# Kernel optimization log

Hardware: AMD Instinct MI355X
Metric: run time of the kernel (lower is better)

Reference implementation:

```python
import jax, jax.numpy as jnp
import numpy as np

N_NODES = 100000
N_EDGES = 1200000
N_GRAPHS = 1024
IN_DIM, HIDDEN, OUT_DIM = 4, 64, 2
BN_EPS = 1e-5


def setup_inputs() -> dict:
    key = jax.random.key(0)
    ks = jax.random.split(key, 12)
    x = jax.random.normal(ks[0], (N_NODES, IN_DIM), dtype=jnp.float32)
    edge_index = jax.random.randint(ks[1], (2, N_EDGES), 0, N_NODES, dtype=jnp.int64)
    batch = jnp.sort(jax.random.randint(ks[2], (N_NODES,), 0, N_GRAPHS, dtype=jnp.int64))
    s = 1.0 / np.sqrt(HIDDEN)
    return {
        "x": x,
        "edge_index": edge_index,
        "batch": batch,
        "W_enc": jax.random.normal(ks[3], (IN_DIM, HIDDEN), dtype=jnp.float32) * 0.5,
        "b_enc": jnp.zeros((HIDDEN,), dtype=jnp.float32),
        "bn_gamma": jnp.ones((HIDDEN,), dtype=jnp.float32),
        "bn_beta": jnp.zeros((HIDDEN,), dtype=jnp.float32),
        "bn_mean": jax.random.normal(ks[4], (HIDDEN,), dtype=jnp.float32) * 0.1,
        "bn_var": jax.random.uniform(ks[5], (HIDDEN,), dtype=jnp.float32, minval=0.5, maxval=1.5),
        "W_gcn": jax.random.normal(ks[6], (HIDDEN, HIDDEN), dtype=jnp.float32) * s,
        "b_gcn": jnp.zeros((HIDDEN,), dtype=jnp.float32),
        "W_cls1": jax.random.normal(ks[7], (HIDDEN, HIDDEN), dtype=jnp.float32) * s,
        "b_cls1": jnp.zeros((HIDDEN,), dtype=jnp.float32),
        "W_cls2": jax.random.normal(ks[8], (HIDDEN, OUT_DIM), dtype=jnp.float32) * s,
        "b_cls2": jnp.zeros((OUT_DIM,), dtype=jnp.float32),
    }


def reference(x, edge_index, batch, W_enc, b_enc, bn_gamma, bn_beta, bn_mean, bn_var,
              W_gcn, b_gcn, W_cls1, b_cls1, W_cls2, b_cls2):
    n = x.shape[0]
    # Encoder: Linear -> ReLU -> Dropout(eval=identity) -> BatchNorm1d (running stats)
    h = jnp.maximum(x @ W_enc + b_enc, 0.0)
    h = (h - bn_mean) * jax.lax.rsqrt(bn_var + BN_EPS) * bn_gamma + bn_beta
    # GCNConv (PyG): add self-loops, symmetric deg^{-1/2} normalization
    loop = jnp.arange(n, dtype=edge_index.dtype)
    src = jnp.concatenate([edge_index[0], loop])  # [E+N]
    dst = jnp.concatenate([edge_index[1], loop])
    deg = jnp.zeros((n,), dtype=h.dtype).at[dst].add(1.0)
    dis = jnp.where(deg > 0, jax.lax.rsqrt(jnp.maximum(deg, 1.0)), 0.0)
    norm = dis[src] * dis[dst]  # [E+N]
    hw = h @ W_gcn  # [N, H]
    msg = hw[src] * norm[:, None]  # gather + scale, [E+N, H]
    agg = jax.ops.segment_sum(msg, dst, num_segments=n) + b_gcn
    agg = jnp.maximum(agg, 0.0)  # .relu()
    # global_mean_pool over graphs
    sums = jax.ops.segment_sum(agg, batch, num_segments=N_GRAPHS)  # [G, H]
    cnts = jax.ops.segment_sum(jnp.ones((n,), dtype=agg.dtype), batch, num_segments=N_GRAPHS)
    gm = sums / jnp.maximum(cnts, 1.0)[:, None]
    # Classifier: Linear -> ReLU -> Dropout(eval) -> Linear
    out = jnp.maximum(gm @ W_cls1 + b_cls1, 0.0) @ W_cls2 + b_cls2
    return out
```

## Files before the change

### kernel.cpp

```cpp
#include <hip/hip_runtime.h>

#define N_NODES  100000
#define N_EDGES  1200000
#define N_GRAPHS 1024

#define BSH    8
#define BNODES 256
#define NBUCK  391
#define BCAP   4096
#define BINB   512
#define CHUNK  ((N_EDGES + BINB - 1) / BINB)
#define ENCB   1563

__device__ __forceinline__ unsigned short f2bf(float f) {
  unsigned u = __float_as_uint(f);
  return (unsigned short)((u + 0x7fffu + ((u >> 16) & 1u)) >> 16);
}
__device__ __forceinline__ float bf2f(unsigned short b) {
  return __uint_as_float(((unsigned)b) << 16);
}

__global__ __launch_bounds__(256) void k_zero(float* __restrict__ gsum,
                                              int* __restrict__ cur,
                                              const int* __restrict__ batch,
                                              float* __restrict__ cnts) {
  int i = blockIdx.x * 256 + threadIdx.x;
  gsum[i] = 0.f;
  if (i < NBUCK) cur[i] = 0;
  if (i < N_GRAPHS) {
    int lo = 0, hi = N_NODES;
    while (lo < hi) { int mid = (lo + hi) >> 1; if (batch[mid] < i) lo = mid + 1; else hi = mid; }
    int lo2 = lo, hi2 = N_NODES;
    while (lo2 < hi2) { int mid = (lo2 + hi2) >> 1; if (batch[mid] < i + 1) lo2 = mid + 1; else hi2 = mid; }
    cnts[i] = fmaxf((float)(lo2 - lo), 1.0f);
  }
}

__global__ __launch_bounds__(256, 2) void k_binenc(
    const int* __restrict__ ei, int* __restrict__ cur, int* __restrict__ binned,
    const float* __restrict__ x,
    const float* __restrict__ Wenc, const float* __restrict__ benc,
    const float* __restrict__ gamma, const float* __restrict__ beta,
    const float* __restrict__ mean,  const float* __restrict__ var,
    const float* __restrict__ Wgcn,
    unsigned short* __restrict__ hw) {
  int t = threadIdx.x;
  int lane = t & 63, w = t >> 6;
  if (blockIdx.x < BINB) {
    __shared__ int h[NBUCK];
    int blk = blockIdx.x;
    for (int i = t; i < NBUCK; i += 256) h[i] = 0;
    __syncthreads();
    int start = blk * CHUNK, end = min(start + CHUNK, N_EDGES);
    for (int e = start + 4 * t; e < end; e += 4 * 256) {
      int4 d4 = *(const int4*)&ei[N_EDGES + e];
      atomicAdd(&h[d4.x >> BSH], 1);
      atomicAdd(&h[d4.y >> BSH], 1);
      atomicAdd(&h[d4.z >> BSH], 1);
      atomicAdd(&h[d4.w >> BSH], 1);
    }
    __syncthreads();
    for (int b = t; b < NBUCK; b += 256) {
      int v = h[b];
      if (v) h[b] = atomicAdd(&cur[b], v);
    }
    __syncthreads();
    for (int e = start + 4 * t; e < end; e += 4 * 256) {
      int4 s4 = *(const int4*)&ei[e];
      int4 d4 = *(const int4*)&ei[N_EDGES + e];
      int b, p;
      b = d4.x >> BSH; p = atomicAdd(&h[b], 1);
      if (p < BCAP) binned[b * BCAP + p] = s4.x | ((d4.x & (BNODES - 1)) << 17);
      b = d4.y >> BSH; p = atomicAdd(&h[b], 1);
      if (p < BCAP) binned[b * BCAP + p] = s4.y | ((d4.y & (BNODES - 1)) << 17);
      b = d4.z >> BSH; p = atomicAdd(&h[b], 1);
      if (p < BCAP) binned[b * BCAP + p] = s4.z | ((d4.z & (BNODES - 1)) << 17);
      b = d4.w >> BSH; p = atomicAdd(&h[b], 1);
      if (p < BCAP) binned[b * BCAP + p] = s4.w | ((d4.w & (BNODES - 1)) << 17);
    }
    return;
  }
  int wv = (blockIdx.x - BINB) * 4 + w;
  if (wv >= 6250) return;
  float be = benc[lane];
  float sc = gamma[lane] * rsqrtf(var[lane] + 1e-5f);
  float mu = mean[lane], bt = beta[lane];
  float w0 = Wenc[lane], w1 = Wenc[64 + lane], w2 = Wenc[128 + lane], w3 = Wenc[192 + lane];
  float wreg[64];
  #pragma unroll
  for (int k = 0; k < 64; ++k) wreg[k] = Wgcn[k * 64 + lane];
  int n0 = wv * 16;
  for (int i = 0; i < 16; ++i) {
    int n = n0 + i;
    float4 xv = ((const float4*)x)[n];
    float h = fmaf(xv.w, w3, fmaf(xv.z, w2, fmaf(xv.y, w1, fmaf(xv.x, w0, be))));
    h = fmaxf(h, 0.f);
    float hbn = (h - mu) * sc + bt;
    int hb = __float_as_int(hbn);
    float a0 = 0.f, a1 = 0.f, a2 = 0.f, a3 = 0.f;
    #pragma unroll
    for (int k = 0; k < 64; k += 4) {
      a0 = fmaf(__int_as_float(__builtin_amdgcn_readlane(hb, k)),     wreg[k],     a0);
      a1 = fmaf(__int_as_float(__builtin_amdgcn_readlane(hb, k + 1)), wreg[k + 1], a1);
      a2 = fmaf(__int_as_float(__builtin_amdgcn_readlane(hb, k + 2)), wreg[k + 2], a2);
      a3 = fmaf(__int_as_float(__builtin_amdgcn_readlane(hb, k + 3)), wreg[k + 3], a3);
    }
    hw[(size_t)n * 64 + lane] = f2bf((a0 + a1) + (a2 + a3));
  }
}

__global__ __launch_bounds__(256) void k_csr(const int* __restrict__ cur,
                                             const int* __restrict__ binned,
                                             int* __restrict__ csr,
                                             unsigned* __restrict__ rowinfo,
                                             float* __restrict__ dis) {
  __shared__ int hist[BNODES];
  __shared__ int wsum[4];
  int t = threadIdx.x, blk = blockIdx.x;
  int lane = t & 63, w = t >> 6;
  int nE = min(cur[blk], BCAP);
  int b0 = blk * BCAP;
  hist[t] = 0;
  __syncthreads();
  for (int i = t; i < nE; i += 256)
    atomicAdd(&hist[(unsigned)binned[b0 + i] >> 17], 1);
  __syncthreads();
  int v = hist[t];
  int incl = v;
  #pragma unroll
  for (int off = 1; off < 64; off <<= 1) {
    int y = __shfl_up(incl, off);
    if (lane >= off) incl += y;
  }
  if (lane == 63) wsum[w] = incl;
  __syncthreads();
  if (t == 0) {
    int s = 0;
    #pragma unroll
    for (int i = 0; i < 4; ++i) { int x2 = wsum[i]; wsum[i] = s; s += x2; }
  }
  __syncthreads();
  int excl = wsum[w] + incl - v;
  hist[t] = excl;
  int node = (blk << BSH) + t;
  if (node < N_NODES) {
    rowinfo[node] = (unsigned)(b0 + excl) | ((unsigned)v << 21);
    dis[node] = rsqrtf((float)(v + 1));
  }
  __syncthreads();
  for (int i = t; i < nE; i += 256) {
    int vv = binned[b0 + i];
    int p = atomicAdd(&hist[(unsigned)vv >> 17], 1);
    csr[b0 + p] = vv & 0x1FFFF;
  }
}

__global__ __launch_bounds__(256) void k_gather(
    const unsigned* __restrict__ rowinfo, const int* __restrict__ csr,
    const float* __restrict__ dis, const unsigned short* __restrict__ hw,
    const int* __restrict__ batch, const float* __restrict__ bgcn,
    float* __restrict__ gsum) {
  int t = threadIdx.x;
  int lane = t & 63, w = t >> 6;
  int nb = blockIdx.x * 16 + w * 4;
  float bias = bgcn[lane];
  float vout[4];
  int gid[4];
  #pragma unroll
  for (int k = 0; k < 4; ++k) {
    int n = nb + k;
    unsigned u = rowinfo[n];
    int st = (int)(u & 0x1FFFFF);
    int v  = (int)(u >> 21);
    int en = st + v;
    float dn = rsqrtf((float)(v + 1));
    float a0 = 0.f, a1 = 0.f, a2 = 0.f, a3 = 0.f;
    float a4 = 0.f, a5 = 0.f, a6 = 0.f, a7 = 0.f;
    for (int c = st; c < en; c += 64) {
      int m = min(64, en - c);
      int idx = c + lane;
      int chunk = 0; float dv = 0.f;
      if (idx < en) { chunk = csr[idx]; dv = dis[chunk]; }
      int dvb = __float_as_int(dv);
      int j = 0;
      for (; j + 8 <= m; j += 8) {
        int s0 = __builtin_amdgcn_readlane(chunk, j);
        int s1 = __builtin_amdgcn_readlane(chunk, j + 1);
        int s2 = __builtin_amdgcn_readlane(chunk, j + 2);
        int s3 = __builtin_amdgcn_readlane(chunk, j + 3);
        int s4 = __builtin_amdgcn_readlane(chunk, j + 4);
        int s5 = __builtin_amdgcn_readlane(chunk, j + 5);
        int s6 = __builtin_amdgcn_readlane(chunk, j + 6);
        int s7 = __builtin_amdgcn_readlane(chunk, j + 7);
        float d0 = __int_as_float(__builtin_amdgcn_readlane(dvb, j));
        float d1 = __int_as_float(__builtin_amdgcn_readlane(dvb, j + 1));
        float d2 = __int_as_float(__builtin_amdgcn_readlane(dvb, j + 2));
        float d3 = __int_as_float(__builtin_amdgcn_readlane(dvb, j + 3));
        float d4 = __int_as_float(__builtin_amdgcn_readlane(dvb, j + 4));
        float d5 = __int_as_float(__builtin_amdgcn_readlane(dvb, j + 5));
        float d6 = __int_as_float(__builtin_amdgcn_readlane(dvb, j + 6));
        float d7 = __int_as_float(__builtin_amdgcn_readlane(dvb, j + 7));
        a0 = fmaf(d0, bf2f(hw[(size_t)s0 * 64 + lane]), a0);
        a1 = fmaf(d1, bf2f(hw[(size_t)s1 * 64 + lane]), a1);
        a2 = fmaf(d2, bf2f(hw[(size_t)s2 * 64 + lane]), a2);
        a3 = fmaf(d3, bf2f(hw[(size_t)s3 * 64 + lane]), a3);
        a4 = fmaf(d4, bf2f(hw[(size_t)s4 * 64 + lane]), a4);
        a5 = fmaf(d5, bf2f(hw[(size_t)s5 * 64 + lane]), a5);
        a6 = fmaf(d6, bf2f(hw[(size_t)s6 * 64 + lane]), a6);
        a7 = fmaf(d7, bf2f(hw[(size_t)s7 * 64 + lane]), a7);
      }
      for (; j + 4 <= m; j += 4) {
        int s0 = __builtin_amdgcn_readlane(chunk, j);
        int s1 = __builtin_amdgcn_readlane(chunk, j + 1);
        int s2 = __builtin_amdgcn_readlane(chunk, j + 2);
        int s3 = __builtin_amdgcn_readlane(chunk, j + 3);
        float d0 = __int_as_float(__builtin_amdgcn_readlane(dvb, j));
        float d1 = __int_as_float(__builtin_amdgcn_readlane(dvb, j + 1));
        float d2 = __int_as_float(__builtin_amdgcn_readlane(dvb, j + 2));
        float d3 = __int_as_float(__builtin_amdgcn_readlane(dvb, j + 3));
        a0 = fmaf(d0, bf2f(hw[(size_t)s0 * 64 + lane]), a0);
        a1 = fmaf(d1, bf2f(hw[(size_t)s1 * 64 + lane]), a1);
        a2 = fmaf(d2, bf2f(hw[(size_t)s2 * 64 + lane]), a2);
        a3 = fmaf(d3, bf2f(hw[(size_t)s3 * 64 + lane]), a3);
      }
      for (; j < m; ++j) {
        int s = __builtin_amdgcn_readlane(chunk, j);
        float d = __int_as_float(__builtin_amdgcn_readlane(dvb, j));
        a0 = fmaf(d, bf2f(hw[(size_t)s * 64 + lane]), a0);
      }
    }
    float self = bf2f(hw[(size_t)n * 64 + lane]);
    float sum = ((a0 + a1) + (a2 + a3)) + ((a4 + a5) + (a6 + a7));
    vout[k] = fmaxf(dn * fmaf(dn, self, sum) + bias, 0.f);
    gid[k] = batch[n];
  }
  float vs = vout[0];
  int cg = gid[0];
  #pragma unroll
  for (int k = 1; k < 4; ++k) {
    if (gid[k] == cg) vs += vout[k];
    else {
      atomicAdd(&gsum[cg * 64 + lane], vs);
      vs = vout[k]; cg = gid[k];
    }
  }
  atomicAdd(&gsum[cg * 64 + lane], vs);
}

__global__ void k_cls(const float* __restrict__ gsum, const float* __restrict__ cnts,
                      const float* __restrict__ W1, const float* __restrict__ b1,
                      const float* __restrict__ W2, const float* __restrict__ b2,
                      float* __restrict__ out) {
  __shared__ float gm[64];
  int j = threadIdx.x;
  int g = blockIdx.x;
  gm[j] = gsum[g * 64 + j] / cnts[g];
  __syncthreads();
  float hid = b1[j];
  #pragma unroll
  for (int k = 0; k < 64; ++k) hid += gm[k] * W1[k * 64 + j];
  hid = fmaxf(hid, 0.f);
  float o0 = hid * W2[j * 2 + 0];
  float o1 = hid * W2[j * 2 + 1];
  #pragma unroll
  for (int off = 32; off > 0; off >>= 1) {
    o0 += __shfl_down(o0, off);
    o1 += __shfl_down(o1, off);
  }
  if (j == 0) {
    out[g * 2 + 0] = o0 + b2[0];
    out[g * 2 + 1] = o1 + b2[1];
  }
}

extern "C" void kernel_launch(void* const* d_in, const int* in_sizes, int n_in,
                              void* d_out, int out_size, void* d_ws, size_t ws_size,
                              hipStream_t stream) {
  const float* x     = (const float*)d_in[0];
  const int*   ei    = (const int*)d_in[1];
  const int*   batch = (const int*)d_in[2];
  const float* Wenc  = (const float*)d_in[3];
  const float* benc  = (const float*)d_in[4];
  const float* gamma = (const float*)d_in[5];
  const float* beta  = (const float*)d_in[6];
  const float* mean  = (const float*)d_in[7];
  const float* var   = (const float*)d_in[8];
  const float* Wgcn  = (const float*)d_in[9];
  const float* bgcn  = (const float*)d_in[10];
  const float* W1    = (const float*)d_in[11];
  const float* b1    = (const float*)d_in[12];
  const float* W2    = (const float*)d_in[13];
  const float* b2    = (const float*)d_in[14];
  float* out = (float*)d_out;

  char* ws = (char*)d_ws;
  float*          gsum    = (float*)ws;          ws += (size_t)N_GRAPHS * 64 * 4;
  int*            cur     = (int*)ws;            ws += (size_t)1024 * 4;
  float*          cnts    = (float*)ws;          ws += (size_t)N_GRAPHS * 4;
  int*            binned  = (int*)ws;            ws += (size_t)NBUCK * BCAP * 4;
  int*            csr     = (int*)ws;            ws += (size_t)NBUCK * BCAP * 4;
  unsigned*       rowinfo = (unsigned*)ws;       ws += (size_t)(N_NODES + 32) * 4;
  float*          dis     = (float*)ws;          ws += (size_t)N_NODES * 4;
  unsigned short* hw      = (unsigned short*)ws; ws += (size_t)N_NODES * 64 * 2;

  k_zero<<<256, 256, 0, stream>>>(gsum, cur, batch, cnts);
  k_binenc<<<BINB + ENCB, 256, 0, stream>>>(ei, cur, binned, x, Wenc, benc,
                                            gamma, beta, mean, var, Wgcn, hw);
  k_csr<<<NBUCK, 256, 0, stream>>>(cur, binned, csr, rowinfo, dis);
  k_gather<<<(N_NODES / 16), 256, 0, stream>>>(rowinfo, csr, dis, hw, batch, bgcn, gsum);
  k_cls<<<N_GRAPHS, 64, 0, stream>>>(gsum, cnts, W1, b1, W2, b2, out);
}
```

Measured before the change: 193.8 us.

## Prescale hw rows by source deg^-1/2 in CSR build, drop dis gather

The source-side normalization factor is folded into hw inside k_csr: each block rescales its 256 nodes' bf16 rows by rsqrt(deg+1) once. The gather kernel then only sums the prescaled rows, which removes the dependent dis[chunk] load and the per-edge readlane/fma of the scale. The gather unroll also drops from 8 to 4 accumulators. In exchange, k_csr does an extra read-modify-write of the whole hw array, and each row is rounded to bf16 a second time, which adds precision error.

After: 208.5 us. 7.6% more time.

```diff
diff --git a/kernel.cpp b/kernel.cpp
--- a/kernel.cpp
+++ b/kernel.cpp
@@ -113,8 +113,9 @@
                                              const int* __restrict__ binned,
                                              int* __restrict__ csr,
                                              unsigned* __restrict__ rowinfo,
-                                             float* __restrict__ dis) {
+                                             unsigned short* __restrict__ hw) {
   __shared__ int hist[BNODES];
+  __shared__ float disS[BNODES];
   __shared__ int wsum[4];
   int t = threadIdx.x, blk = blockIdx.x;
   int lane = t & 63, w = t >> 6;
@@ -142,12 +143,19 @@
   __syncthreads();
   int excl = wsum[w] + incl - v;
   hist[t] = excl;
+  disS[t] = rsqrtf((float)(v + 1));
   int node = (blk << BSH) + t;
-  if (node < N_NODES) {
+  if (node < N_NODES)
     rowinfo[node] = (unsigned)(b0 + excl) | ((unsigned)v << 21);
-    dis[node] = rsqrtf((float)(v + 1));
-  }
-  __syncthreads();
+  __syncthreads();
+  int base = blk << BSH;
+  for (int r = w * 64; r < w * 64 + 64; ++r) {
+    int n = base + r;
+    if (n >= N_NODES) break;
+    float d = disS[r];
+    size_t off = (size_t)n * 64 + lane;
+    hw[off] = f2bf(bf2f(hw[off]) * d);
+  }
   for (int i = t; i < nE; i += 256) {
     int vv = binned[b0 + i];
     int p = atomicAdd(&hist[(unsigned)vv >> 17], 1);
@@ -157,7 +165,7 @@
 
 __global__ __launch_bounds__(256) void k_gather(
     const unsigned* __restrict__ rowinfo, const int* __restrict__ csr,
-    const float* __restrict__ dis, const unsigned short* __restrict__ hw,
+    const unsigned short* __restrict__ hw,
     const int* __restrict__ batch, const float* __restrict__ bgcn,
     float* __restrict__ gsum) {
   int t = threadIdx.x;
@@ -175,63 +183,29 @@
     int en = st + v;
     float dn = rsqrtf((float)(v + 1));
     float a0 = 0.f, a1 = 0.f, a2 = 0.f, a3 = 0.f;
-    float a4 = 0.f, a5 = 0.f, a6 = 0.f, a7 = 0.f;
     for (int c = st; c < en; c += 64) {
       int m = min(64, en - c);
       int idx = c + lane;
-      int chunk = 0; float dv = 0.f;
-      if (idx < en) { chunk = csr[idx]; dv = dis[chunk]; }
-      int dvb = __float_as_int(dv);
+      int chunk = (idx < en) ? csr[idx] : 0;
       int j = 0;
-      for (; j + 8 <= m; j += 8) {
-        int s0 = __builtin_amdgcn_readlane(chunk, j);
-        int s1 = __builtin_amdgcn_readlane(chunk, j + 1);
-        int s2 = __builtin_amdgcn_readlane(chunk, j + 2);
-        int s3 = __builtin_amdgcn_readlane(chunk, j + 3);
-        int s4 = __builtin_amdgcn_readlane(chunk, j + 4);
-        int s5 = __builtin_amdgcn_readlane(chunk, j + 5);
-        int s6 = __builtin_amdgcn_readlane(chunk, j + 6);
-        int s7 = __builtin_amdgcn_readlane(chunk, j + 7);
-        float d0 = __int_as_float(__builtin_amdgcn_readlane(dvb, j));
-        float d1 = __int_as_float(__builtin_amdgcn_readlane(dvb, j + 1));
-        float d2 = __int_as_float(__builtin_amdgcn_readlane(dvb, j + 2));
-        float d3 = __int_as_float(__builtin_amdgcn_readlane(dvb, j + 3));
-        float d4 = __int_as_float(__builtin_amdgcn_readlane(dvb, j + 4));
-        float d5 = __int_as_float(__builtin_amdgcn_readlane(dvb, j + 5));
-        float d6 = __int_as_float(__builtin_amdgcn_readlane(dvb, j + 6));
-        float d7 = __int_as_float(__builtin_amdgcn_readlane(dvb, j + 7));
-        a0 = fmaf(d0, bf2f(hw[(size_t)s0 * 64 + lane]), a0);
-        a1 = fmaf(d1, bf2f(hw[(size_t)s1 * 64 + lane]), a1);
-        a2 = fmaf(d2, bf2f(hw[(size_t)s2 * 64 + lane]), a2);
-        a3 = fmaf(d3, bf2f(hw[(size_t)s3 * 64 + lane]), a3);
-        a4 = fmaf(d4, bf2f(hw[(size_t)s4 * 64 + lane]), a4);
-        a5 = fmaf(d5, bf2f(hw[(size_t)s5 * 64 + lane]), a5);
-        a6 = fmaf(d6, bf2f(hw[(size_t)s6 * 64 + lane]), a6);
-        a7 = fmaf(d7, bf2f(hw[(size_t)s7 * 64 + lane]), a7);
-      }
       for (; j + 4 <= m; j += 4) {
         int s0 = __builtin_amdgcn_readlane(chunk, j);
         int s1 = __builtin_amdgcn_readlane(chunk, j + 1);
         int s2 = __builtin_amdgcn_readlane(chunk, j + 2);
         int s3 = __builtin_amdgcn_readlane(chunk, j + 3);
-        float d0 = __int_as_float(__builtin_amdgcn_readlane(dvb, j));
-        float d1 = __int_as_float(__builtin_amdgcn_readlane(dvb, j + 1));
-        float d2 = __int_as_float(__builtin_amdgcn_readlane(dvb, j + 2));
-        float d3 = __int_as_float(__builtin_amdgcn_readlane(dvb, j + 3));
-        a0 = fmaf(d0, bf2f(hw[(size_t)s0 * 64 + lane]), a0);
-        a1 = fmaf(d1, bf2f(hw[(size_t)s1 * 64 + lane]), a1);
-        a2 = fmaf(d2, bf2f(hw[(size_t)s2 * 64 + lane]), a2);
-        a3 = fmaf(d3, bf2f(hw[(size_t)s3 * 64 + lane]), a3);
+        a0 += bf2f(hw[(size_t)s0 * 64 + lane]);
+        a1 += bf2f(hw[(size_t)s1 * 64 + lane]);
+        a2 += bf2f(hw[(size_t)s2 * 64 + lane]);
+        a3 += bf2f(hw[(size_t)s3 * 64 + lane]);
       }
       for (; j < m; ++j) {
         int s = __builtin_amdgcn_readlane(chunk, j);
-        float d = __int_as_float(__builtin_amdgcn_readlane(dvb, j));
-        a0 = fmaf(d, bf2f(hw[(size_t)s * 64 + lane]), a0);
+        a0 += bf2f(hw[(size_t)s * 64 + lane]);
       }
     }
     float self = bf2f(hw[(size_t)n * 64 + lane]);
-    float sum = ((a0 + a1) + (a2 + a3)) + ((a4 + a5) + (a6 + a7));
-    vout[k] = fmaxf(dn * fmaf(dn, self, sum) + bias, 0.f);
+    float sum = ((a0 + a1) + (a2 + a3)) + self;
+    vout[k] = fmaxf(fmaf(dn, sum, bias), 0.f);
     gid[k] = batch[n];
   }
   float vs = vout[0];
@@ -300,13 +274,12 @@
   int*            binned  = (int*)ws;            ws += (size_t)NBUCK * BCAP * 4;
   int*            csr     = (int*)ws;            ws += (size_t)NBUCK * BCAP * 4;
   unsigned*       rowinfo = (unsigned*)ws;       ws += (size_t)(N_NODES + 32) * 4;
-  float*          dis     = (float*)ws;          ws += (size_t)N_NODES * 4;
   unsigned short* hw      = (unsigned short*)ws; ws += (size_t)N_NODES * 64 * 2;
 
   k_zero<<<256, 256, 0, stream>>>(gsum, cur, batch, cnts);
   k_binenc<<<BINB + ENCB, 256, 0, stream>>>(ei, cur, binned, x, Wenc, benc,
                                             gamma, beta, mean, var, Wgcn, hw);
-  k_csr<<<NBUCK, 256, 0, stream>>>(cur, binned, csr, rowinfo, dis);
-  k_gather<<<(N_NODES / 16), 256, 0, stream>>>(rowinfo, csr, dis, hw, batch, bgcn, gsum);
+  k_csr<<<NBUCK, 256, 0, stream>>>(cur, binned, csr, rowinfo, hw);
+  k_gather<<<(N_NODES / 16), 256, 0, stream>>>(rowinfo, csr, hw, batch, bgcn, gsum);
   k_cls<<<N_GRAPHS, 64, 0, stream>>>(gsum, cnts, W1, b1, W2, b2, out);
 }
```
